# Kernel tuning notes

Measured on AMD Instinct MI355X. Metric: run time of the kernel, lower is better.

## Reference

```python
import jax, jax.numpy as jnp
import numpy as np

BN_EPS = 1e-5


def _lin(key, fan_in, fan_out):
    k1, k2 = jax.random.split(key)
    s = 1.0 / np.sqrt(fan_in)
    w = jax.random.uniform(k1, (fan_in, fan_out), jnp.float32, -s, s)
    b = jax.random.uniform(k2, (fan_out,), jnp.float32, -s, s)
    return w, b


def setup_inputs() -> dict:
    key = jax.random.key(0)
    ks = jax.random.split(key, 24)
    N, E, F_IN, E_DIM, G = 50000, 800000, 64, 16, 128
    inp = {}
    inp["x"] = jax.random.normal(ks[0], (N, F_IN), jnp.float32)
    inp["edge_attr"] = jax.random.normal(ks[1], (E, E_DIM), jnp.float32)
    inp["edge_index"] = jax.random.randint(ks[2], (2, E), 0, N, jnp.int64)
    inp["batch_ids"] = jnp.sort(jax.random.randint(ks[3], (N,), 0, G, jnp.int64))
    # conv1: edge lin (16->64), mlp 64->256->256
    inp["we1"], inp["be1"] = _lin(ks[4], E_DIM, F_IN)
    inp["w1a"], inp["b1a"] = _lin(ks[5], F_IN, 256)
    inp["w1b"], inp["b1b"] = _lin(ks[6], 256, 256)
    inp["bn1_g"] = jnp.ones((256,), jnp.float32)
    inp["bn1_b"] = jnp.zeros((256,), jnp.float32)
    inp["bn1_m"] = 0.1 * jax.random.normal(ks[7], (256,), jnp.float32)
    inp["bn1_v"] = jnp.abs(jax.random.normal(ks[8], (256,), jnp.float32)) + 0.5
    # conv2: edge lin (16->256), mlp 256->128->128
    inp["we2"], inp["be2"] = _lin(ks[9], E_DIM, 256)
    inp["w2a"], inp["b2a"] = _lin(ks[10], 256, 128)
    inp["w2b"], inp["b2b"] = _lin(ks[11], 128, 128)
    inp["bn2_g"] = jnp.ones((128,), jnp.float32)
    inp["bn2_b"] = jnp.zeros((128,), jnp.float32)
    inp["bn2_m"] = 0.1 * jax.random.normal(ks[12], (128,), jnp.float32)
    inp["bn2_v"] = jnp.abs(jax.random.normal(ks[13], (128,), jnp.float32)) + 0.5
    # conv3: edge lin (16->128), mlp 128->64->64
    inp["we3"], inp["be3"] = _lin(ks[14], E_DIM, 128)
    inp["w3a"], inp["b3a"] = _lin(ks[15], 128, 64)
    inp["w3b"], inp["b3b"] = _lin(ks[16], 64, 64)
    inp["bn3_g"] = jnp.ones((64,), jnp.float32)
    inp["bn3_b"] = jnp.zeros((64,), jnp.float32)
    inp["bn3_m"] = 0.1 * jax.random.normal(ks[17], (64,), jnp.float32)
    inp["bn3_v"] = jnp.abs(jax.random.normal(ks[18], (64,), jnp.float32)) + 0.5
    inp["fc1_w"], inp["fc1_b"] = _lin(ks[19], 64, 16)
    inp["fc2_w"], inp["fc2_b"] = _lin(ks[20], 16, 1)
    return inp


def _gine(x, edge_index, edge_attr, we, be, wa, ba, wb, bb):
    # GINEConv, eps=0: mlp(x + sum_j relu(x_j + lin_e(e_ji)))
    src, dst = edge_index[0], edge_index[1]
    msg = jax.nn.relu(x[src] + edge_attr @ we + be)  # [E, d]
    agg = jax.ops.segment_sum(msg, dst, num_segments=x.shape[0])
    h = x + agg
    return jax.nn.relu(h @ wa + ba) @ wb + bb


def _bn(x, g, b, m, v):
    return (x - m) * jax.lax.rsqrt(v + BN_EPS) * g + b


def reference(x, edge_attr, edge_index, batch_ids,
              we1, be1, w1a, b1a, w1b, b1b, bn1_g, bn1_b, bn1_m, bn1_v,
              we2, be2, w2a, b2a, w2b, b2b, bn2_g, bn2_b, bn2_m, bn2_v,
              we3, be3, w3a, b3a, w3b, b3b, bn3_g, bn3_b, bn3_m, bn3_v,
              fc1_w, fc1_b, fc2_w, fc2_b):
    G = 128  # num graphs
    h = _gine(x, edge_index, edge_attr, we1, be1, w1a, b1a, w1b, b1b)
    h = _bn(jax.nn.relu(h), bn1_g, bn1_b, bn1_m, bn1_v)
    h = _gine(h, edge_index, edge_attr, we2, be2, w2a, b2a, w2b, b2b)
    h = _bn(jax.nn.relu(h), bn2_g, bn2_b, bn2_m, bn2_v)
    h = _gine(h, edge_index, edge_attr, we3, be3, w3a, b3a, w3b, b3b)
    h = _bn(jax.nn.relu(h), bn3_g, bn3_b, bn3_m, bn3_v)
    pooled = jax.ops.segment_sum(h, batch_ids, num_segments=G)  # [G, 64]
    out = jax.nn.relu(pooled @ fc1_w + fc1_b) @ fc2_w + fc2_b  # [G, 1]
    return out
```

## Files before the change

### kernel.cpp

```cpp
#include <hip/hip_runtime.h>
#include <hip/hip_bf16.h>

#define BN_EPS 1e-5f

typedef __attribute__((ext_vector_type(8))) short short8v;
typedef __attribute__((ext_vector_type(4))) float f32x4;
typedef _Float16 f16x2 __attribute__((ext_vector_type(2)));
typedef __hip_bfloat16 bf16;
typedef unsigned short ushort_t;
typedef unsigned int uint_t;

__global__ void count_kernel(const int* __restrict__ dst, int* __restrict__ deg,
                             int E, int N) {
    int i = blockIdx.x * blockDim.x + threadIdx.x;
    if (i >= E) return;
    int d = dst[i];
    d = min(max(d, 0), N - 1);
    atomicAdd(&deg[d], 1);
}

__global__ __launch_bounds__(256) void scan1_kernel(const int* __restrict__ deg,
                                                    int* __restrict__ bsum, int N) {
    int t = threadIdx.x, b = blockIdx.x;
    int i = b * 256 + t;
    int v = (i < N) ? deg[i] : 0;
#pragma unroll
    for (int d = 32; d; d >>= 1) v += __shfl_xor(v, d, 64);
    __shared__ int ws[4];
    if ((t & 63) == 0) ws[t >> 6] = v;
    __syncthreads();
    if (t == 0) bsum[b] = ws[0] + ws[1] + ws[2] + ws[3];
}

__global__ __launch_bounds__(256) void scan3_kernel(const int* __restrict__ deg,
                                                    const int* __restrict__ bsum,
                                                    int* __restrict__ off,
                                                    int* __restrict__ cur,
                                                    int N, int nb) {
    int t = threadIdx.x, b = blockIdx.x;
    int lane = t & 63, w = t >> 6;

    int partial = 0;
    for (int j = t; j < b; j += 256) partial += bsum[j];
#pragma unroll
    for (int d = 32; d; d >>= 1) partial += __shfl_xor(partial, d, 64);
    __shared__ int bsm[4];
    if (lane == 0) bsm[w] = partial;
    __syncthreads();
    int base = bsm[0] + bsm[1] + bsm[2] + bsm[3];

    int i = b * 256 + t;
    int v = (i < N) ? deg[i] : 0;
    int inc = v;
#pragma unroll
    for (int d = 1; d < 64; d <<= 1) {
        int u = __shfl_up(inc, d, 64);
        if (lane >= d) inc += u;
    }
    __shared__ int ws[4];
    if (lane == 63) ws[w] = inc;
    __syncthreads();
    for (int j = 0; j < w; ++j) base += ws[j];
    int excl = base + inc - v;
    if (i < N) { off[i] = excl; cur[i] = excl; }
    if (i == N - 1) off[N] = excl + v;
}

__global__ void fill_kernel(const int* __restrict__ src, const int* __restrict__ dst,
                            const float* __restrict__ ea, int* __restrict__ cur,
                            int* __restrict__ srcs, uint_t* __restrict__ each,
                            int E, int N) {
    int i = blockIdx.x * blockDim.x + threadIdx.x;
    if (i >= E) return;
    int d = dst[i];
    d = min(max(d, 0), N - 1);
    int p = atomicAdd(&cur[d], 1);
    srcs[p] = min(max(src[i], 0), N - 1);
    uint_t pk[8];
#pragma unroll
    for (int q = 0; q < 4; ++q) {
        float4 a = *(const float4*)&ea[(size_t)i * 16 + q * 4];
        f16x2 h0 = {(_Float16)a.x, (_Float16)a.y};
        f16x2 h1 = {(_Float16)a.z, (_Float16)a.w};
        pk[q * 2 + 0] = __builtin_bit_cast(uint_t, h0);
        pk[q * 2 + 1] = __builtin_bit_cast(uint_t, h1);
    }
    *(uint4*)&each[(size_t)p * 8 + 0] = *(uint4*)&pk[0];
    *(uint4*)&each[(size_t)p * 8 + 4] = *(uint4*)&pk[4];
}

__global__ void megaconv_kernel(
    const float* __restrict__ x, bf16* __restrict__ xb, int nx4,
    const float* __restrict__ w1a, const float* __restrict__ w1b,
    const float* __restrict__ w2a, const float* __restrict__ w2b,
    const float* __restrict__ w3a, const float* __restrict__ w3b,
    bf16* __restrict__ wt,
    const float* __restrict__ we1, const float* __restrict__ we2,
    const float* __restrict__ we3, uint_t* __restrict__ wef,
    int* __restrict__ deg, int N, float* __restrict__ pooled) {
    int t = blockIdx.x * blockDim.x + threadIdx.x;
    if (t < nx4) {
        int i = t * 4;
        float4 v = *(const float4*)&x[i];
        xb[i + 0] = __float2bfloat16(v.x);
        xb[i + 1] = __float2bfloat16(v.y);
        xb[i + 2] = __float2bfloat16(v.z);
        xb[i + 3] = __float2bfloat16(v.w);
        return;
    }
    t -= nx4;
    if (t < 143360) {
        const float* w; int K, Nc, base, r;
        if (t < 16384)       { w = w1a; K = 64;  Nc = 256; base = 0;      r = t; }
        else if (t < 81920)  { w = w1b; K = 256; Nc = 256; base = 16384;  r = t - 16384; }
        else if (t < 114688) { w = w2a; K = 256; Nc = 128; base = 81920;  r = t - 81920; }
        else if (t < 131072) { w = w2b; K = 128; Nc = 128; base = 114688; r = t - 114688; }
        else if (t < 139264) { w = w3a; K = 128; Nc = 64;  base = 131072; r = t - 131072; }
        else                 { w = w3b; K = 64;  Nc = 64;  base = 139264; r = t - 139264; }
        int k = r % K, n = r / K;
        wt[base + r] = __float2bfloat16(w[(size_t)k * Nc + n]);
        return;
    }
    t -= 143360;
    if (t < 3584) {
        const float* w; int D, base, r;
        if (t < 512)        { w = we1; D = 64;  base = 0;    r = t; }
        else if (t < 2560)  { w = we2; D = 256; base = 512;  r = t - 512; }
        else                { w = we3; D = 128; base = 2560; r = t - 2560; }
        int p = r / D, col = r % D;
        f16x2 h = {(_Float16)w[(size_t)(2 * p) * D + col],
                   (_Float16)w[(size_t)(2 * p + 1) * D + col]};
        wef[base + r] = __builtin_bit_cast(uint_t, h);
        return;
    }
    t -= 3584;
    {
        int nd4 = (N + 3) / 4;
        if (t < nd4) {
            int i = t * 4;
#pragma unroll
            for (int j = 0; j < 4; ++j)
                if (i + j < N) deg[i + j] = 0;
            return;
        }
        t -= nd4;
        if (t < 2048) {
            *(float4*)&pooled[t * 4] = make_float4(0.f, 0.f, 0.f, 0.f);
        }
    }
}

template <int C>
__global__ __launch_bounds__(256) void msg_fused(
    const uint_t* __restrict__ each, const int* __restrict__ srcs,
    const int* __restrict__ off, const bf16* __restrict__ x,
    const uint_t* __restrict__ wef, const float* __restrict__ be,
    bf16* __restrict__ t, int N) {
    constexpr int D = C * 64;
    const int lane = threadIdx.x & 63;
    const int n = blockIdx.x * 4 + (threadIdx.x >> 6);
    if (n >= N) return;
    const int col0 = lane * C;

    uint_t wreg[8][C];
#pragma unroll
    for (int p = 0; p < 8; ++p)
#pragma unroll
        for (int c = 0; c < C; ++c) wreg[p][c] = wef[p * D + col0 + c];
    float breg[C];
#pragma unroll
    for (int c = 0; c < C; ++c) breg[c] = be[col0 + c];

    float acc[C];
#pragma unroll
    for (int c = 0; c < C; ++c) acc[c] = 0.f;

    const ushort_t* xp = (const ushort_t*)x;

    const int i0 = __builtin_amdgcn_readfirstlane(off[n]);
    const int i1 = __builtin_amdgcn_readfirstlane(off[n + 1]);

#define BF2F(u) (__builtin_bit_cast(float, (unsigned)(u) << 16))
#define H2(u) (__builtin_bit_cast(f16x2, u))

    int i = i0;
    int sN[4] = {0, 0, 0, 0};
    if (i + 4 <= i1) {
#pragma unroll
        for (int j = 0; j < 4; ++j)
            sN[j] = __builtin_amdgcn_readfirstlane(srcs[i + j]);
    }
    for (; i + 4 <= i1; i += 4) {
        int s[4];
#pragma unroll
        for (int j = 0; j < 4; ++j) s[j] = sN[j];
        ushort_t xv[4][C];
#pragma unroll
        for (int j = 0; j < 4; ++j) {
            if constexpr (C == 4) {
                *(ushort4*)xv[j] = *(const ushort4*)&xp[(size_t)s[j] * D + col0];
            } else if constexpr (C == 2) {
                *(ushort2*)xv[j] = *(const ushort2*)&xp[(size_t)s[j] * D + col0];
            } else {
                xv[j][0] = xp[(size_t)s[j] * D + col0];
            }
        }
        if (i + 8 <= i1) {
#pragma unroll
            for (int j = 0; j < 4; ++j)
                sN[j] = __builtin_amdgcn_readfirstlane(srcs[i + 4 + j]);
        }
        uint_t e[4][8];
#pragma unroll
        for (int j = 0; j < 4; ++j)
#pragma unroll
            for (int p = 0; p < 8; ++p) e[j][p] = each[(size_t)(i + j) * 8 + p];

        float m[4][C];
#pragma unroll
        for (int j = 0; j < 4; ++j)
#pragma unroll
            for (int c = 0; c < C; ++c)
                m[j][c] = __builtin_amdgcn_fdot2(H2(e[j][0]), H2(wreg[0][c]), breg[c], false);
#pragma unroll
        for (int p = 1; p < 8; ++p)
#pragma unroll
            for (int j = 0; j < 4; ++j)
#pragma unroll
                for (int c = 0; c < C; ++c)
                    m[j][c] = __builtin_amdgcn_fdot2(H2(e[j][p]), H2(wreg[p][c]), m[j][c], false);
#pragma unroll
        for (int j = 0; j < 4; ++j)
#pragma unroll
            for (int c = 0; c < C; ++c)
                acc[c] += fmaxf(m[j][c] + BF2F(xv[j][c]), 0.f);
    }
    for (; i < i1; ++i) {
        const int s0 = __builtin_amdgcn_readfirstlane(srcs[i]);
        ushort_t xv0[C];
        if constexpr (C == 4) {
            *(ushort4*)xv0 = *(const ushort4*)&xp[(size_t)s0 * D + col0];
        } else if constexpr (C == 2) {
            *(ushort2*)xv0 = *(const ushort2*)&xp[(size_t)s0 * D + col0];
        } else {
            xv0[0] = xp[(size_t)s0 * D + col0];
        }
        uint_t e0[8];
#pragma unroll
        for (int p = 0; p < 8; ++p) e0[p] = each[(size_t)i * 8 + p];
        float m0[C];
#pragma unroll
        for (int c = 0; c < C; ++c)
            m0[c] = __builtin_amdgcn_fdot2(H2(e0[0]), H2(wreg[0][c]), breg[c], false);
#pragma unroll
        for (int p = 1; p < 8; ++p)
#pragma unroll
            for (int c = 0; c < C; ++c)
                m0[c] = __builtin_amdgcn_fdot2(H2(e0[p]), H2(wreg[p][c]), m0[c], false);
#pragma unroll
        for (int c = 0; c < C; ++c) acc[c] += fmaxf(m0[c] + BF2F(xv0[c]), 0.f);
    }

#pragma unroll
    for (int c = 0; c < C; ++c) {
        float xo = BF2F(xp[(size_t)n * D + col0 + c]);
        t[(size_t)n * D + col0 + c] = __float2bfloat16(xo + acc[c]);
    }
#undef BF2F
#undef H2
}

template <int H, int NC>
__global__ __launch_bounds__(256) void mlp_fused(
    const bf16* __restrict__ A, const bf16* __restrict__ W1t,
    const float* __restrict__ b1, const bf16* __restrict__ W2t,
    const float* __restrict__ b2, const float* __restrict__ bng,
    const float* __restrict__ bnb, const float* __restrict__ bnm,
    const float* __restrict__ bnv, bf16* __restrict__ C,
    const int* __restrict__ batch, float* __restrict__ pooled,
    int M, int K1, int mode) {
    constexpr int NT1 = H / 16;
    constexpr int NT2 = NC / 16;
    constexpr int LDH = H + 8;
    __shared__ __align__(16) ushort_t u_lds[128 * LDH];

    const int lane = threadIdx.x & 63;
    const int w = threadIdx.x >> 6;
    const int r16 = lane & 15;
    const int kg = lane >> 4;
    const int mbase = blockIdx.x * 128 + w * 32;
    const int lbase = w * 32;

    const short* Ap = (const short*)A;
    const short* W1p = (const short*)W1t;
    const short* W2p = (const short*)W2t;

    {
        f32x4 acc[2][NT1];
#pragma unroll
        for (int f = 0; f < 2; ++f)
#pragma unroll
            for (int nt = 0; nt < NT1; ++nt) acc[f][nt] = (f32x4){0.f, 0.f, 0.f, 0.f};

        for (int k0 = 0; k0 < K1; k0 += 32) {
            short8v a0 = *(const short8v*)&Ap[(size_t)(mbase + r16) * K1 + k0 + kg * 8];
            short8v a1 = *(const short8v*)&Ap[(size_t)(mbase + 16 + r16) * K1 + k0 + kg * 8];
#pragma unroll
            for (int nt = 0; nt < NT1; ++nt) {
                short8v b = *(const short8v*)&W1p[(size_t)(nt * 16 + r16) * K1 + k0 + kg * 8];
                acc[0][nt] = __builtin_amdgcn_mfma_f32_16x16x32_bf16(a0, b, acc[0][nt], 0, 0, 0);
                acc[1][nt] = __builtin_amdgcn_mfma_f32_16x16x32_bf16(a1, b, acc[1][nt], 0, 0, 0);
            }
        }
#pragma unroll
        for (int nt = 0; nt < NT1; ++nt) {
            int col = nt * 16 + r16;
            float bs = b1[col];
#pragma unroll
            for (int f = 0; f < 2; ++f) {
#pragma unroll
                for (int rg = 0; rg < 4; ++rg) {
                    int rl = lbase + f * 16 + kg * 4 + rg;
                    float z = fmaxf(acc[f][nt][rg] + bs, 0.f);
                    u_lds[rl * LDH + col] =
                        __builtin_bit_cast(ushort_t, __float2bfloat16(z));
                }
            }
        }
    }
    __syncthreads();

    f32x4 acc2[2][NT2];
#pragma unroll
    for (int f = 0; f < 2; ++f)
#pragma unroll
        for (int nt = 0; nt < NT2; ++nt) acc2[f][nt] = (f32x4){0.f, 0.f, 0.f, 0.f};

    for (int k0 = 0; k0 < H; k0 += 32) {
        short8v a0 = *(const short8v*)&u_lds[(lbase + r16) * LDH + k0 + kg * 8];
        short8v a1 = *(const short8v*)&u_lds[(lbase + 16 + r16) * LDH + k0 + kg * 8];
#pragma unroll
        for (int nt = 0; nt < NT2; ++nt) {
            short8v b = *(const short8v*)&W2p[(size_t)(nt * 16 + r16) * H + k0 + kg * 8];
            acc2[0][nt] = __builtin_amdgcn_mfma_f32_16x16x32_bf16(a0, b, acc2[0][nt], 0, 0, 0);
            acc2[1][nt] = __builtin_amdgcn_mfma_f32_16x16x32_bf16(a1, b, acc2[1][nt], 0, 0, 0);
        }
    }

    float bs[NT2], sc[NT2], sh[NT2];
#pragma unroll
    for (int nt = 0; nt < NT2; ++nt) {
        int col = nt * 16 + r16;
        bs[nt] = b2[col];
        sc[nt] = rsqrtf(bnv[col] + BN_EPS) * bng[col];
        sh[nt] = bnb[col] - bnm[col] * sc[nt];
    }

#pragma unroll
    for (int f = 0; f < 2; ++f) {
#pragma unroll
        for (int rg = 0; rg < 4; ++rg) {
            int row = mbase + f * 16 + kg * 4 + rg;
            if (row >= M) continue;
            int g = 0;
            if (mode == 3) g = min(max(batch[row], 0), 127);
#pragma unroll
            for (int nt = 0; nt < NT2; ++nt) {
                int col = nt * 16 + r16;
                float z = fmaxf(acc2[f][nt][rg] + bs[nt], 0.f);
                z = z * sc[nt] + sh[nt];
                if (mode == 3)
                    atomicAdd(&pooled[g * NC + col], z);
                else
                    C[(size_t)row * NC + col] = __float2bfloat16(z);
            }
        }
    }
}

__global__ __launch_bounds__(128) void head_kernel(
    const float* __restrict__ pooled, const float* __restrict__ w1,
    const float* __restrict__ b1, const float* __restrict__ w2,
    const float* __restrict__ b2, float* __restrict__ out) {
    const int g = threadIdx.x;
    float p[64];
#pragma unroll
    for (int i = 0; i < 64; ++i) p[i] = pooled[g * 64 + i];
    float o = b2[0];
#pragma unroll
    for (int j = 0; j < 16; ++j) {
        float hsum = b1[j];
#pragma unroll
        for (int i = 0; i < 64; ++i) hsum = fmaf(p[i], w1[i * 16 + j], hsum);
        o = fmaf(fmaxf(hsum, 0.f), w2[j], o);
    }
    out[g] = o;
}

extern "C" void kernel_launch(void* const* d_in, const int* in_sizes, int n_in,
                              void* d_out, int out_size, void* d_ws,
                              size_t ws_size, hipStream_t stream) {
    const float* x     = (const float*)d_in[0];
    const float* ea    = (const float*)d_in[1];
    const int*   ei    = (const int*)d_in[2];
    const int*   batch = (const int*)d_in[3];
    const float* we1 = (const float*)d_in[4];
    const float* be1 = (const float*)d_in[5];
    const float* w1a = (const float*)d_in[6];
    const float* b1a = (const float*)d_in[7];
    const float* w1b = (const float*)d_in[8];
    const float* b1b = (const float*)d_in[9];
    const float* bn1g = (const float*)d_in[10];
    const float* bn1b = (const float*)d_in[11];
    const float* bn1m = (const float*)d_in[12];
    const float* bn1v = (const float*)d_in[13];
    const float* we2 = (const float*)d_in[14];
    const float* be2 = (const float*)d_in[15];
    const float* w2a = (const float*)d_in[16];
    const float* b2a = (const float*)d_in[17];
    const float* w2b = (const float*)d_in[18];
    const float* b2b = (const float*)d_in[19];
    const float* bn2g = (const float*)d_in[20];
    const float* bn2b = (const float*)d_in[21];
    const float* bn2m = (const float*)d_in[22];
    const float* bn2v = (const float*)d_in[23];
    const float* we3 = (const float*)d_in[24];
    const float* be3 = (const float*)d_in[25];
    const float* w3a = (const float*)d_in[26];
    const float* b3a = (const float*)d_in[27];
    const float* w3b = (const float*)d_in[28];
    const float* b3b = (const float*)d_in[29];
    const float* bn3g = (const float*)d_in[30];
    const float* bn3b = (const float*)d_in[31];
    const float* bn3m = (const float*)d_in[32];
    const float* bn3v = (const float*)d_in[33];
    const float* fc1w = (const float*)d_in[34];
    const float* fc1b = (const float*)d_in[35];
    const float* fc2w = (const float*)d_in[36];
    const float* fc2b = (const float*)d_in[37];

    const int N = in_sizes[0] / 64;
    const int E = in_sizes[1] / 16;
    const int M_pad = ((N + 127) / 128) * 128;
    const int* src = ei;
    const int* dst = ei + E;

    char* wsp = (char*)d_ws;
    auto alloc = [&](size_t bytes) -> void* {
        void* p = (void*)wsp;
        wsp += (bytes + 255) & ~(size_t)255;
        return p;
    };
    const int nb = (N + 255) / 256;
    int* deg    = (int*)alloc((size_t)N * 4);
    int* off    = (int*)alloc((size_t)(N + 1) * 4);
    int* cur    = (int*)alloc((size_t)N * 4);
    int* bsum   = (int*)alloc((size_t)nb * 4);
    int* srcs   = (int*)alloc((size_t)E * 4);
    uint_t* each = (uint_t*)alloc((size_t)E * 8 * 4);
    bf16* xb    = (bf16*)alloc((size_t)N * 64 * 2);
    bf16* tb    = (bf16*)alloc((size_t)M_pad * 256 * 2);
    bf16* hb    = (bf16*)alloc((size_t)M_pad * 256 * 2);
    bf16* wt    = (bf16*)alloc((size_t)143360 * 2);
    uint_t* wef = (uint_t*)alloc((size_t)3584 * 4);
    float* pooled = (float*)alloc(128 * 64 * 4);

    bf16* wt1a = wt + 0;
    bf16* wt1b = wt + 16384;
    bf16* wt2a = wt + 81920;
    bf16* wt2b = wt + 114688;
    bf16* wt3a = wt + 131072;
    bf16* wt3b = wt + 139264;
    uint_t* wef1 = wef + 0;
    uint_t* wef2 = wef + 512;
    uint_t* wef3 = wef + 2560;

    {
        int nx4 = N * 64 / 4;
        int total = nx4 + 143360 + 3584 + (N + 3) / 4 + 2048;
        megaconv_kernel<<<(total + 255) / 256, 256, 0, stream>>>(
            x, xb, nx4, w1a, w1b, w2a, w2b, w3a, w3b, wt, we1, we2, we3, wef,
            deg, N, pooled);
    }

    int eb = (E + 255) / 256;
    count_kernel<<<eb, 256, 0, stream>>>(dst, deg, E, N);
    scan1_kernel<<<nb, 256, 0, stream>>>(deg, bsum, N);
    scan3_kernel<<<nb, 256, 0, stream>>>(deg, bsum, off, cur, N, nb);
    fill_kernel<<<eb, 256, 0, stream>>>(src, dst, ea, cur, srcs, each, E, N);

    const int gblk = M_pad / 128;
    const int mblk = (N + 3) / 4;

    msg_fused<1><<<mblk, 256, 0, stream>>>(each, srcs, off, xb, wef1, be1, tb, N);
    mlp_fused<256, 256><<<gblk, 256, 0, stream>>>(tb, wt1a, b1a, wt1b, b1b,
                                                  bn1g, bn1b, bn1m, bn1v,
                                                  hb, nullptr, nullptr, N, 64, 2);
    msg_fused<4><<<mblk, 256, 0, stream>>>(each, srcs, off, hb, wef2, be2, tb, N);
    mlp_fused<128, 128><<<gblk, 256, 0, stream>>>(tb, wt2a, b2a, wt2b, b2b,
                                                  bn2g, bn2b, bn2m, bn2v,
                                                  hb, nullptr, nullptr, N, 256, 2);
    msg_fused<2><<<mblk, 256, 0, stream>>>(each, srcs, off, hb, wef3, be3, tb, N);
    mlp_fused<64, 64><<<gblk, 256, 0, stream>>>(tb, wt3a, b3a, wt3b, b3b,
                                                bn3g, bn3b, bn3m, bn3v,
                                                nullptr, batch, pooled, N, 128, 3);

    head_kernel<<<1, 128, 0, stream>>>(pooled, fc1w, fc1b, fc2w, fc2b, (float*)d_out);
}
```

Baseline: 445.5 us.

## Split fused two-layer MLP kernel into separate tiled GEMM launches

Replaces the fused MLP kernel, which kept the hidden activation in LDS, with a generic 64x64-tile MFMA GEMM kernel launched twice per layer. The intermediate activation now goes through a new global buffer ub. The 2D grid gives many more, smaller blocks and drops the large LDS allocation, which should raise occupancy and parallelism. The cost is extra global traffic for the intermediate, three more launches, and the A tile being reloaded once per column block.

After: 505.1 us. +13.4%, slower.

```diff
diff --git a/kernel.cpp b/kernel.cpp
--- a/kernel.cpp
+++ b/kernel.cpp
@@ -270,110 +270,65 @@
 #undef H2
 }
 
-template <int H, int NC>
-__global__ __launch_bounds__(256) void mlp_fused(
-    const bf16* __restrict__ A, const bf16* __restrict__ W1t,
-    const float* __restrict__ b1, const bf16* __restrict__ W2t,
-    const float* __restrict__ b2, const float* __restrict__ bng,
+template <int NC>
+__global__ __launch_bounds__(256) void gemm16(
+    const bf16* __restrict__ A, const bf16* __restrict__ Wt,
+    const float* __restrict__ bias, const float* __restrict__ bng,
     const float* __restrict__ bnb, const float* __restrict__ bnm,
     const float* __restrict__ bnv, bf16* __restrict__ C,
     const int* __restrict__ batch, float* __restrict__ pooled,
-    int M, int K1, int mode) {
-    constexpr int NT1 = H / 16;
-    constexpr int NT2 = NC / 16;
-    constexpr int LDH = H + 8;
-    __shared__ __align__(16) ushort_t u_lds[128 * LDH];
-
+    int M, int K, int mode) {
     const int lane = threadIdx.x & 63;
     const int w = threadIdx.x >> 6;
     const int r16 = lane & 15;
     const int kg = lane >> 4;
-    const int mbase = blockIdx.x * 128 + w * 32;
-    const int lbase = w * 32;
+    const int mbase = blockIdx.x * 64 + w * 16;
+    const int nbase = blockIdx.y * 64;
+
+    f32x4 acc[4];
+#pragma unroll
+    for (int nt = 0; nt < 4; ++nt) acc[nt] = (f32x4){0.f, 0.f, 0.f, 0.f};
 
     const short* Ap = (const short*)A;
-    const short* W1p = (const short*)W1t;
-    const short* W2p = (const short*)W2t;
-
-    {
-        f32x4 acc[2][NT1];
-#pragma unroll
-        for (int f = 0; f < 2; ++f)
-#pragma unroll
-            for (int nt = 0; nt < NT1; ++nt) acc[f][nt] = (f32x4){0.f, 0.f, 0.f, 0.f};
-
-        for (int k0 = 0; k0 < K1; k0 += 32) {
-            short8v a0 = *(const short8v*)&Ap[(size_t)(mbase + r16) * K1 + k0 + kg * 8];
-            short8v a1 = *(const short8v*)&Ap[(size_t)(mbase + 16 + r16) * K1 + k0 + kg * 8];
-#pragma unroll
-            for (int nt = 0; nt < NT1; ++nt) {
-                short8v b = *(const short8v*)&W1p[(size_t)(nt * 16 + r16) * K1 + k0 + kg * 8];
-                acc[0][nt] = __builtin_amdgcn_mfma_f32_16x16x32_bf16(a0, b, acc[0][nt], 0, 0, 0);
-                acc[1][nt] = __builtin_amdgcn_mfma_f32_16x16x32_bf16(a1, b, acc[1][nt], 0, 0, 0);
-            }
-        }
-#pragma unroll
-        for (int nt = 0; nt < NT1; ++nt) {
-            int col = nt * 16 + r16;
-            float bs = b1[col];
-#pragma unroll
-            for (int f = 0; f < 2; ++f) {
-#pragma unroll
-                for (int rg = 0; rg < 4; ++rg) {
-                    int rl = lbase + f * 16 + kg * 4 + rg;
-                    float z = fmaxf(acc[f][nt][rg] + bs, 0.f);
-                    u_lds[rl * LDH + col] =
-                        __builtin_bit_cast(ushort_t, __float2bfloat16(z));
-                }
-            }
-        }
-    }
-    __syncthreads();
-
-    f32x4 acc2[2][NT2];
-#pragma unroll
-    for (int f = 0; f < 2; ++f)
-#pragma unroll
-        for (int nt = 0; nt < NT2; ++nt) acc2[f][nt] = (f32x4){0.f, 0.f, 0.f, 0.f};
-
-    for (int k0 = 0; k0 < H; k0 += 32) {
-        short8v a0 = *(const short8v*)&u_lds[(lbase + r16) * LDH + k0 + kg * 8];
-        short8v a1 = *(const short8v*)&u_lds[(lbase + 16 + r16) * LDH + k0 + kg * 8];
-#pragma unroll
-        for (int nt = 0; nt < NT2; ++nt) {
-            short8v b = *(const short8v*)&W2p[(size_t)(nt * 16 + r16) * H + k0 + kg * 8];
-            acc2[0][nt] = __builtin_amdgcn_mfma_f32_16x16x32_bf16(a0, b, acc2[0][nt], 0, 0, 0);
-            acc2[1][nt] = __builtin_amdgcn_mfma_f32_16x16x32_bf16(a1, b, acc2[1][nt], 0, 0, 0);
-        }
-    }
-
-    float bs[NT2], sc[NT2], sh[NT2];
-#pragma unroll
-    for (int nt = 0; nt < NT2; ++nt) {
-        int col = nt * 16 + r16;
-        bs[nt] = b2[col];
-        sc[nt] = rsqrtf(bnv[col] + BN_EPS) * bng[col];
-        sh[nt] = bnb[col] - bnm[col] * sc[nt];
-    }
-
-#pragma unroll
-    for (int f = 0; f < 2; ++f) {
-#pragma unroll
-        for (int rg = 0; rg < 4; ++rg) {
-            int row = mbase + f * 16 + kg * 4 + rg;
-            if (row >= M) continue;
-            int g = 0;
-            if (mode == 3) g = min(max(batch[row], 0), 127);
-#pragma unroll
-            for (int nt = 0; nt < NT2; ++nt) {
-                int col = nt * 16 + r16;
-                float z = fmaxf(acc2[f][nt][rg] + bs[nt], 0.f);
-                z = z * sc[nt] + sh[nt];
-                if (mode == 3)
-                    atomicAdd(&pooled[g * NC + col], z);
-                else
-                    C[(size_t)row * NC + col] = __float2bfloat16(z);
-            }
+    const short* Wp = (const short*)Wt;
+
+    for (int k0 = 0; k0 < K; k0 += 32) {
+        short8v a = *(const short8v*)&Ap[(size_t)(mbase + r16) * K + k0 + kg * 8];
+#pragma unroll
+        for (int nt = 0; nt < 4; ++nt) {
+            short8v b = *(const short8v*)&Wp[(size_t)(nbase + nt * 16 + r16) * K + k0 + kg * 8];
+            acc[nt] = __builtin_amdgcn_mfma_f32_16x16x32_bf16(a, b, acc[nt], 0, 0, 0);
+        }
+    }
+
+    float bs[4], sc[4], sh[4];
+#pragma unroll
+    for (int nt = 0; nt < 4; ++nt) {
+        int col = nbase + nt * 16 + r16;
+        bs[nt] = bias[col];
+        sc[nt] = 1.f; sh[nt] = 0.f;
+        if (mode >= 2) {
+            sc[nt] = rsqrtf(bnv[col] + BN_EPS) * bng[col];
+            sh[nt] = bnb[col] - bnm[col] * sc[nt];
+        }
+    }
+
+#pragma unroll
+    for (int rg = 0; rg < 4; ++rg) {
+        int row = mbase + kg * 4 + rg;
+        if (row >= M) continue;
+        int g = 0;
+        if (mode == 3) g = min(max(batch[row], 0), 127);
+#pragma unroll
+        for (int nt = 0; nt < 4; ++nt) {
+            int col = nbase + nt * 16 + r16;
+            float z = acc[nt][rg] + bs[nt];
+            z = fmaxf(z, 0.f);
+            if (mode >= 2) z = z * sc[nt] + sh[nt];
+            if (mode == 3)
+                atomicAdd(&pooled[g * NC + col], z);
+            else
+                C[(size_t)row * NC + col] = __float2bfloat16(z);
         }
     }
 }
@@ -441,7 +396,7 @@
 
     const int N = in_sizes[0] / 64;
     const int E = in_sizes[1] / 16;
-    const int M_pad = ((N + 127) / 128) * 128;
+    const int M_pad = ((N + 63) / 64) * 64;
     const int* src = ei;
     const int* dst = ei + E;
 
@@ -458,8 +413,9 @@
     int* bsum   = (int*)alloc((size_t)nb * 4);
     int* srcs   = (int*)alloc((size_t)E * 4);
     uint_t* each = (uint_t*)alloc((size_t)E * 8 * 4);
-    bf16* xb    = (bf16*)alloc((size_t)N * 64 * 2);
+    bf16* xb    = (bf16*)alloc((size_t)M_pad * 64 * 2);
     bf16* tb    = (bf16*)alloc((size_t)M_pad * 256 * 2);
+    bf16* ub    = (bf16*)alloc((size_t)M_pad * 256 * 2);
     bf16* hb    = (bf16*)alloc((size_t)M_pad * 256 * 2);
     bf16* wt    = (bf16*)alloc((size_t)143360 * 2);
     uint_t* wef = (uint_t*)alloc((size_t)3584 * 4);
@@ -489,21 +445,30 @@
     scan3_kernel<<<nb, 256, 0, stream>>>(deg, bsum, off, cur, N, nb);
     fill_kernel<<<eb, 256, 0, stream>>>(src, dst, ea, cur, srcs, each, E, N);
 
-    const int gblk = M_pad / 128;
+    const int g64 = M_pad / 64;
     const int mblk = (N + 3) / 4;
 
     msg_fused<1><<<mblk, 256, 0, stream>>>(each, srcs, off, xb, wef1, be1, tb, N);
-    mlp_fused<256, 256><<<gblk, 256, 0, stream>>>(tb, wt1a, b1a, wt1b, b1b,
-                                                  bn1g, bn1b, bn1m, bn1v,
-                                                  hb, nullptr, nullptr, N, 64, 2);
+    gemm16<256><<<dim3(g64, 4), 256, 0, stream>>>(tb, wt1a, b1a, nullptr, nullptr,
+                                                  nullptr, nullptr, ub, nullptr,
+                                                  nullptr, N, 64, 1);
+    gemm16<256><<<dim3(g64, 4), 256, 0, stream>>>(ub, wt1b, b1b, bn1g, bn1b, bn1m,
+                                                  bn1v, hb, nullptr, nullptr,
+                                                  N, 256, 2);
     msg_fused<4><<<mblk, 256, 0, stream>>>(each, srcs, off, hb, wef2, be2, tb, N);
-    mlp_fused<128, 128><<<gblk, 256, 0, stream>>>(tb, wt2a, b2a, wt2b, b2b,
-                                                  bn2g, bn2b, bn2m, bn2v,
-                                                  hb, nullptr, nullptr, N, 256, 2);
+    gemm16<128><<<dim3(g64, 2), 256, 0, stream>>>(tb, wt2a, b2a, nullptr, nullptr,
+                                                  nullptr, nullptr, ub, nullptr,
+                                                  nullptr, N, 256, 1);
+    gemm16<128><<<dim3(g64, 2), 256, 0, stream>>>(ub, wt2b, b2b, bn2g, bn2b, bn2m,
+                                                  bn2v, hb, nullptr, nullptr,
+                                                  N, 128, 2);
     msg_fused<2><<<mblk, 256, 0, stream>>>(each, srcs, off, hb, wef3, be3, tb, N);
-    mlp_fused<64, 64><<<gblk, 256, 0, stream>>>(tb, wt3a, b3a, wt3b, b3b,
-                                                bn3g, bn3b, bn3m, bn3v,
-                                                nullptr, batch, pooled, N, 128, 3);
+    gemm16<64><<<dim3(g64, 1), 256, 0, stream>>>(tb, wt3a, b3a, nullptr, nullptr,
+                                                 nullptr, nullptr, ub, nullptr,
+                                                 nullptr, N, 128, 1);
+    gemm16<64><<<dim3(g64, 1), 256, 0, stream>>>(ub, wt3b, b3b, bn3g, bn3b, bn3m,
+                                                 bn3v, nullptr, batch, pooled,
+                                                 N, 64, 3);
 
     head_kernel<<<1, 128, 0, stream>>>(pooled, fc1w, fc1b, fc2w, fc2b, (float*)d_out);
 }
```
